# Kernel optimization log

Measured on AMD Instinct MI355X. Metric: run time of the kernel, lower is better.

Reference implementation:

```python
import jax, jax.numpy as jnp
import numpy as np

N_CAP = 10000   # self.n default: >= bs so the [:, :n] slice is a no-op
MARGIN = 0.3    # forward default m


def setup_inputs() -> dict:
    key = jax.random.key(0)
    k1, k2 = jax.random.split(key)
    bs, dim = 2048, 256
    sketch = jax.random.normal(k1, (bs, dim), dtype=jnp.float32)
    photo = jax.random.normal(k2, (bs, dim), dtype=jnp.float32)
    return {"sketch": sketch, "photo": photo}


def reference(sketch, photo):
    # d == 2 branch: Euclidean distances.
    bs = sketch.shape[0]
    # positive distance per row: ||sketch_i - photo_i||_2  -> (bs,)
    pos = jnp.sqrt(jnp.sum((sketch - photo) ** 2, axis=1))
    # negative distance matrix neg[i, j] = ||sketch_j - photo_i||_2  -> (bs, bs)
    # GEMM identity instead of materializing the (bs,bs,dim) broadcast:
    # ||a-b||^2 = ||a||^2 + ||b||^2 - 2 a.b  (same math, fused/efficient form)
    sn = jnp.sum(sketch ** 2, axis=1)            # (bs,)
    pn = jnp.sum(photo ** 2, axis=1)             # (bs,)
    cross = jnp.einsum('id,jd->ij', photo, sketch)  # (bs, bs): photo rows x sketch cols
    neg2 = jnp.maximum(pn[:, None] + sn[None, :] - 2.0 * cross, 0.0)
    neg = jnp.sqrt(neg2)
    # triplet: pos broadcasts as a row vector (pos[j] - neg[i,j]) + m
    tl = pos[None, :] - neg + MARGIN
    # zero the diagonal, relu, column-cap, then mean over dim 1 and overall
    eye = jnp.eye(bs, dtype=tl.dtype)
    tl = jax.nn.relu(tl * (1.0 - eye))
    tl = tl[:, :N_CAP]
    return jnp.mean(jnp.mean(tl, axis=1))
```

## Files before the change

kernel.cpp:

```cpp
#include <hip/hip_runtime.h>

#define BS 2048
#define DIM 256
#define MARGIN_F 0.3f
#define NBLK 1024

typedef __attribute__((ext_vector_type(4))) float f32x4;
typedef __attribute__((ext_vector_type(2))) __fp16 fp16x2;
typedef __attribute__((ext_vector_type(8))) _Float16 f16x8;

__device__ __forceinline__ void gload_lds16(const void* g, void* l) {
    __builtin_amdgcn_global_load_lds((const __attribute__((address_space(1))) void*)g,
                                     (__attribute__((address_space(3))) void*)l,
                                     16, 0, 0);
}

__global__ __launch_bounds__(256) void tl_prep(const float* __restrict__ sketch,
                                               const float* __restrict__ photo,
                                               float* __restrict__ sn,
                                               float* __restrict__ pn,
                                               float* __restrict__ pos,
                                               _Float16* __restrict__ hs,
                                               _Float16* __restrict__ hp) {
    const int t = threadIdx.x;
    const int w = t >> 6, lane = t & 63;
    const int row = blockIdx.x * 4 + w;
    const float4 s4 = *reinterpret_cast<const float4*>(&sketch[(size_t)row * DIM + lane * 4]);
    const float4 p4 = *reinterpret_cast<const float4*>(&photo [(size_t)row * DIM + lane * 4]);

    float vs = s4.x * s4.x + s4.y * s4.y + s4.z * s4.z + s4.w * s4.w;
    float vp = p4.x * p4.x + p4.y * p4.y + p4.z * p4.z + p4.w * p4.w;
    float dx = s4.x - p4.x, dy = s4.y - p4.y, dz = s4.z - p4.z, dw = s4.w - p4.w;
    float vd = dx * dx + dy * dy + dz * dz + dw * dw;
    #pragma unroll
    for (int off = 32; off > 0; off >>= 1) {
        vs += __shfl_down(vs, off);
        vp += __shfl_down(vp, off);
        vd += __shfl_down(vd, off);
    }
    if (lane == 0) { sn[row] = vs; pn[row] = vp; pos[row] = sqrtf(vd); }

    union { fp16x2 h2[2]; uint2 u; } cs, cp;
    cs.h2[0] = __builtin_amdgcn_cvt_pkrtz(s4.x, s4.y);
    cs.h2[1] = __builtin_amdgcn_cvt_pkrtz(s4.z, s4.w);
    cp.h2[0] = __builtin_amdgcn_cvt_pkrtz(p4.x, p4.y);
    cp.h2[1] = __builtin_amdgcn_cvt_pkrtz(p4.z, p4.w);
    const int qg = lane >> 1;
    const int pg = (qg & 24) | ((qg & 7) ^ (row & 7));
    const size_t dsth = (size_t)row * DIM + pg * 8 + (lane & 1) * 4;
    *reinterpret_cast<uint2*>(&hs[dsth]) = cs.u;
    *reinterpret_cast<uint2*>(&hp[dsth]) = cp.u;
}

__global__ __launch_bounds__(256) void tl_gemm(const _Float16* __restrict__ hp,
                                               const _Float16* __restrict__ hs,
                                               const float* __restrict__ sn,
                                               const float* __restrict__ pn,
                                               const float* __restrict__ pos,
                                               float* __restrict__ partials) {
    __shared__ _Float16 As[64][64];
    __shared__ _Float16 Bs[64][64];

    const int t = threadIdx.x;
    const int i0 = blockIdx.y * 64;
    const int j0 = blockIdx.x * 64;
    const int w = t >> 6, lane = t & 63;
    const int wr = (w >> 1) * 32;
    const int wc = (w & 1) * 32;
    const int r16 = lane & 15, g = lane >> 4;

    f32x4 acc00 = {}, acc01 = {}, acc10 = {}, acc11 = {};

    const int srow = w * 16 + (lane >> 3);
    const int sch  = lane & 7;
    const _Float16* gA0 = &hp[(size_t)(i0 + srow) * DIM + sch * 8];
    const _Float16* gB0 = &hs[(size_t)(j0 + srow) * DIM + sch * 8];
    const _Float16* gA1 = gA0 + 8 * DIM;
    const _Float16* gB1 = gB0 + 8 * DIM;
    _Float16* lA0 = &As[w * 16][0];
    _Float16* lA1 = &As[w * 16 + 8][0];
    _Float16* lB0 = &Bs[w * 16][0];
    _Float16* lB1 = &Bs[w * 16 + 8][0];

    const int xa = (r16 & 7);
    const _Float16* rA0 = &As[wr + r16][0];
    const _Float16* rA1 = &As[wr + 16 + r16][0];
    const _Float16* rB0 = &Bs[wc + r16][0];
    const _Float16* rB1 = &Bs[wc + 16 + r16][0];

    #pragma unroll 1
    for (int kw = 0; kw < 4; ++kw) {
        const int koff = kw * 64;
        gload_lds16(gA0 + koff, lA0);
        gload_lds16(gA1 + koff, lA1);
        gload_lds16(gB0 + koff, lB0);
        gload_lds16(gB1 + koff, lB1);
        __syncthreads();
        #pragma unroll 1
        for (int ks = 0; ks < 2; ++ks) {
            const int q8 = ((ks * 4 + g) ^ xa) * 8;
            f16x8 a0 = *reinterpret_cast<const f16x8*>(rA0 + q8);
            f16x8 a1 = *reinterpret_cast<const f16x8*>(rA1 + q8);
            f16x8 b0 = *reinterpret_cast<const f16x8*>(rB0 + q8);
            f16x8 b1 = *reinterpret_cast<const f16x8*>(rB1 + q8);
            acc00 = __builtin_amdgcn_mfma_f32_16x16x32_f16(a0, b0, acc00, 0, 0, 0);
            acc01 = __builtin_amdgcn_mfma_f32_16x16x32_f16(a0, b1, acc01, 0, 0, 0);
            acc10 = __builtin_amdgcn_mfma_f32_16x16x32_f16(a1, b0, acc10, 0, 0, 0);
            acc11 = __builtin_amdgcn_mfma_f32_16x16x32_f16(a1, b1, acc11, 0, 0, 0);
        }
        __syncthreads();
    }

    const int jl = r16;
    const int rl = g * 4;
    float partial = 0.0f;

    #pragma unroll
    for (int n = 0; n < 2; ++n) {
        const int j = j0 + wc + n * 16 + jl;
        const float snj = sn[j];
        const float posj = pos[j];
        const f32x4 cn0 = (n == 0) ? acc00 : acc01;
        const f32x4 cn1 = (n == 0) ? acc10 : acc11;
        #pragma unroll
        for (int m = 0; m < 2; ++m) {
            const int ibase = i0 + wr + m * 16 + rl;
            const f32x4 cv = (m == 0) ? cn0 : cn1;
            #pragma unroll
            for (int r = 0; r < 4; ++r) {
                const int i = ibase + r;
                const float c = cv[r];
                float neg2 = fmaxf(pn[i] + snj - 2.0f * c, 0.0f);
                float tl = posj - sqrtf(neg2) + MARGIN_F;
                partial += (i != j) ? fmaxf(tl, 0.0f) : 0.0f;
            }
        }
    }

    #pragma unroll
    for (int off = 32; off > 0; off >>= 1) partial += __shfl_down(partial, off);
    __shared__ float lsum[4];
    if (lane == 0) lsum[w] = partial;
    __syncthreads();
    if (t == 0)
        partials[blockIdx.y * 32 + blockIdx.x] = lsum[0] + lsum[1] + lsum[2] + lsum[3];
}

__global__ __launch_bounds__(256) void tl_reduce(const float* __restrict__ partials,
                                                 float* __restrict__ out) {
    const int t = threadIdx.x;
    const float4 v = reinterpret_cast<const float4*>(partials)[t];
    float s = v.x + v.y + v.z + v.w;
    #pragma unroll
    for (int off = 32; off > 0; off >>= 1) s += __shfl_down(s, off);
    __shared__ float lsum[4];
    const int w = t >> 6, lane = t & 63;
    if (lane == 0) lsum[w] = s;
    __syncthreads();
    if (t == 0)
        out[0] = (lsum[0] + lsum[1] + lsum[2] + lsum[3]) * (1.0f / ((float)BS * (float)BS));
}

extern "C" void kernel_launch(void* const* d_in, const int* in_sizes, int n_in,
                              void* d_out, int out_size, void* d_ws, size_t ws_size,
                              hipStream_t stream) {
    const float* sketch = (const float*)d_in[0];
    const float* photo  = (const float*)d_in[1];
    float* out = (float*)d_out;

    float* sn  = (float*)d_ws;
    float* pn  = sn + BS;
    float* pos = pn + BS;
    _Float16* hp = (_Float16*)(pos + BS);
    _Float16* hs = hp + (size_t)BS * DIM;
    float* partials = (float*)(hs + (size_t)BS * DIM);

    tl_prep<<<dim3(BS / 4), dim3(256), 0, stream>>>(sketch, photo, sn, pn, pos, hs, hp);

    dim3 grid(BS / 64, BS / 64);
    tl_gemm<<<grid, dim3(256), 0, stream>>>(hp, hs, sn, pn, pos, partials);

    tl_reduce<<<dim3(1), dim3(256), 0, stream>>>(partials, out);
}
```

Baseline: 18.61 us.

## Load full K panel into LDS at once and remap blocks per XCD

```diff
diff --git a/kernel.cpp b/kernel.cpp
--- a/kernel.cpp
+++ b/kernel.cpp
@@ -3,7 +3,6 @@
 #define BS 2048
 #define DIM 256
 #define MARGIN_F 0.3f
-#define NBLK 1024
 
 typedef __attribute__((ext_vector_type(4))) float f32x4;
 typedef __attribute__((ext_vector_type(2))) __fp16 fp16x2;
@@ -58,12 +57,17 @@
                                                const float* __restrict__ pn,
                                                const float* __restrict__ pos,
                                                float* __restrict__ partials) {
-    __shared__ _Float16 As[64][64];
-    __shared__ _Float16 Bs[64][64];
+    __shared__ _Float16 As[4][64][64];
+    __shared__ _Float16 Bs[4][64][64];
+
+    const int b = blockIdx.x;
+    const int xcd = b & 7, slot = b >> 3;
+    const int by = (xcd & 3) * 8 + (slot >> 4);
+    const int bx = (xcd >> 2) * 16 + (slot & 15);
 
     const int t = threadIdx.x;
-    const int i0 = blockIdx.y * 64;
-    const int j0 = blockIdx.x * 64;
+    const int i0 = by * 64;
+    const int j0 = bx * 64;
     const int w = t >> 6, lane = t & 63;
     const int wr = (w >> 1) * 32;
     const int wc = (w & 1) * 32;
@@ -75,40 +79,32 @@
     const int sch  = lane & 7;
     const _Float16* gA0 = &hp[(size_t)(i0 + srow) * DIM + sch * 8];
     const _Float16* gB0 = &hs[(size_t)(j0 + srow) * DIM + sch * 8];
-    const _Float16* gA1 = gA0 + 8 * DIM;
-    const _Float16* gB1 = gB0 + 8 * DIM;
-    _Float16* lA0 = &As[w * 16][0];
-    _Float16* lA1 = &As[w * 16 + 8][0];
-    _Float16* lB0 = &Bs[w * 16][0];
-    _Float16* lB1 = &Bs[w * 16 + 8][0];
 
-    const int xa = (r16 & 7);
-    const _Float16* rA0 = &As[wr + r16][0];
-    const _Float16* rA1 = &As[wr + 16 + r16][0];
-    const _Float16* rB0 = &Bs[wc + r16][0];
-    const _Float16* rB1 = &Bs[wc + 16 + r16][0];
-
-    #pragma unroll 1
+    #pragma unroll
     for (int kw = 0; kw < 4; ++kw) {
         const int koff = kw * 64;
-        gload_lds16(gA0 + koff, lA0);
-        gload_lds16(gA1 + koff, lA1);
-        gload_lds16(gB0 + koff, lB0);
-        gload_lds16(gB1 + koff, lB1);
-        __syncthreads();
-        #pragma unroll 1
+        gload_lds16(gA0 + koff,           &As[kw][w * 16][0]);
+        gload_lds16(gA0 + 8 * DIM + koff, &As[kw][w * 16 + 8][0]);
+        gload_lds16(gB0 + koff,           &Bs[kw][w * 16][0]);
+        gload_lds16(gB0 + 8 * DIM + koff, &Bs[kw][w * 16 + 8][0]);
+    }
+    __syncthreads();
+
+    const int xa = r16 & 7;
+    #pragma unroll
+    for (int kw = 0; kw < 4; ++kw) {
+        #pragma unroll
         for (int ks = 0; ks < 2; ++ks) {
             const int q8 = ((ks * 4 + g) ^ xa) * 8;
-            f16x8 a0 = *reinterpret_cast<const f16x8*>(rA0 + q8);
-            f16x8 a1 = *reinterpret_cast<const f16x8*>(rA1 + q8);
-            f16x8 b0 = *reinterpret_cast<const f16x8*>(rB0 + q8);
-            f16x8 b1 = *reinterpret_cast<const f16x8*>(rB1 + q8);
+            f16x8 a0 = *reinterpret_cast<const f16x8*>(&As[kw][wr + r16][q8]);
+            f16x8 a1 = *reinterpret_cast<const f16x8*>(&As[kw][wr + 16 + r16][q8]);
+            f16x8 b0 = *reinterpret_cast<const f16x8*>(&Bs[kw][wc + r16][q8]);
+            f16x8 b1 = *reinterpret_cast<const f16x8*>(&Bs[kw][wc + 16 + r16][q8]);
             acc00 = __builtin_amdgcn_mfma_f32_16x16x32_f16(a0, b0, acc00, 0, 0, 0);
             acc01 = __builtin_amdgcn_mfma_f32_16x16x32_f16(a0, b1, acc01, 0, 0, 0);
             acc10 = __builtin_amdgcn_mfma_f32_16x16x32_f16(a1, b0, acc10, 0, 0, 0);
             acc11 = __builtin_amdgcn_mfma_f32_16x16x32_f16(a1, b1, acc11, 0, 0, 0);
         }
-        __syncthreads();
     }
 
     const int jl = r16;
@@ -143,7 +139,7 @@
     if (lane == 0) lsum[w] = partial;
     __syncthreads();
     if (t == 0)
-        partials[blockIdx.y * 32 + blockIdx.x] = lsum[0] + lsum[1] + lsum[2] + lsum[3];
+        partials[b] = lsum[0] + lsum[1] + lsum[2] + lsum[3];
 }
 
 __global__ __launch_bounds__(256) void tl_reduce(const float* __restrict__ partials,
@@ -177,8 +173,7 @@
 
     tl_prep<<<dim3(BS / 4), dim3(256), 0, stream>>>(sketch, photo, sn, pn, pos, hs, hp);
 
-    dim3 grid(BS / 64, BS / 64);
-    tl_gemm<<<grid, dim3(256), 0, stream>>>(hp, hs, sn, pn, pos, partials);
+    tl_gemm<<<dim3(1024), dim3(256), 0, stream>>>(hp, hs, sn, pn, pos, partials);
 
     tl_reduce<<<dim3(1), dim3(256), 0, stream>>>(partials, out);
 }
```

Result: slower. 19.60 us (+5.3%).
